# Optimization experiments

Measured on AMD Instinct MI355X. Metric: run time of the kernel, lower is better.

## Reference

```python
import jax, jax.numpy as jnp
import numpy as np

N_NODE = 50000
N_EDGE = 640000
IN_DIM = 128
OUT_DIM = 128
ATTN_DIM = 128
N_REL = 500
REL_VOCAB = 2 * N_REL + 3  # 1003


def setup_inputs() -> dict:
    key = jax.random.key(0)
    ks = jax.random.split(key, 10)
    hidden = jax.random.normal(ks[0], (N_NODE, IN_DIM), dtype=jnp.float32)
    sub = jax.random.randint(ks[1], (N_EDGE,), 0, N_NODE)
    rel = jax.random.randint(ks[2], (N_EDGE,), 0, REL_VOCAB)
    obj = jax.random.randint(ks[3], (N_EDGE,), 0, N_NODE)
    zero = jnp.zeros((N_EDGE,), dtype=jnp.int64 if jax.config.read('jax_enable_x64') else jnp.int32)
    # edges layout: [:,2]=rel, [:,4]=sub, [:,5]=obj (other columns unused)
    edges = jnp.stack([zero, zero, rel, zero, sub, obj], axis=1)
    old_nodes_new_idx = jax.random.randint(ks[4], (N_NODE,), 0, N_NODE)
    s = 1.0 / np.sqrt(IN_DIM)
    rela_embed = jax.random.normal(ks[5], (REL_VOCAB, IN_DIM), dtype=jnp.float32)
    Ws_attn = jax.random.uniform(ks[6], (IN_DIM, ATTN_DIM), minval=-s, maxval=s, dtype=jnp.float32)
    Wr_attn = jax.random.uniform(ks[7], (IN_DIM, ATTN_DIM), minval=-s, maxval=s, dtype=jnp.float32)
    sa = 1.0 / np.sqrt(ATTN_DIM)
    w_alpha_w = jax.random.uniform(ks[8], (ATTN_DIM, 1), minval=-sa, maxval=sa, dtype=jnp.float32)
    w_alpha_b = jnp.zeros((1,), dtype=jnp.float32)
    W_h = jax.random.uniform(ks[9], (IN_DIM, OUT_DIM), minval=-s, maxval=s, dtype=jnp.float32)
    return {
        'hidden': hidden, 'edges': edges, 'n_node': N_NODE,
        'old_nodes_new_idx': old_nodes_new_idx,
        'rela_embed': rela_embed, 'Ws_attn': Ws_attn, 'Wr_attn': Wr_attn,
        'w_alpha_w': w_alpha_w, 'w_alpha_b': w_alpha_b, 'W_h': W_h,
    }


def reference(hidden, edges, n_node, old_nodes_new_idx,
              rela_embed, Ws_attn, Wr_attn, w_alpha_w, w_alpha_b, W_h):
    sub = edges[:, 4]
    rel = edges[:, 2]
    obj = edges[:, 5]
    hs = hidden[sub]                 # [E, in_dim] gather
    hr = rela_embed[rel]             # [E, in_dim] gather
    message = hs + hr                # [E, in_dim]
    attn_h = jax.nn.relu(hs @ Ws_attn + hr @ Wr_attn)          # [E, attn_dim]
    alpha = jax.nn.sigmoid(attn_h @ w_alpha_w + w_alpha_b)     # [E, 1]
    message = alpha * message
    message_agg = jax.ops.segment_sum(message, obj, num_segments=n_node)  # [N, in_dim]
    hidden_new = message_agg @ W_h   # act is identity by default
    return hidden_new
```

## Files before the change

### kernel.cpp

```cpp
#include <hip/hip_runtime.h>

typedef float f4 __attribute__((ext_vector_type(4)));
typedef float f2 __attribute__((ext_vector_type(2)));
typedef float f8 __attribute__((ext_vector_type(8)));
typedef float f32x4 __attribute__((ext_vector_type(4)));
typedef short bf16x8 __attribute__((ext_vector_type(8)));
typedef unsigned short u16x8 __attribute__((ext_vector_type(8)));

__device__ inline float bf2f(unsigned short u) {
  return __uint_as_float(((unsigned)u) << 16);
}
__device__ inline unsigned short f2bf(float f) {
  unsigned u = __float_as_uint(f);
  return (unsigned short)((u + 0x7FFF + ((u >> 16) & 1)) >> 16);
}

__global__ __launch_bounds__(256) void prep(
    const float* __restrict__ Ws, const float* __restrict__ Wr,
    const float* __restrict__ Wh, const int* __restrict__ edges, int n_edge,
    unsigned short* __restrict__ WsT, unsigned short* __restrict__ WrT,
    unsigned short* __restrict__ WhT, int* __restrict__ counts) {
  const int t = threadIdx.x;
  int b = blockIdx.x;
  if (b < 192) {
    int wsel = b >> 6;
    const float* W = wsel == 0 ? Ws : (wsel == 1 ? Wr : Wh);
    unsigned short* WT = wsel == 0 ? WsT : (wsel == 1 ? WrT : WhT);
    int e = (b & 63) * 256 + t;
    int cc = e >> 7, kk = e & 127;
    WT[e] = f2bf(W[kk * 128 + cc]);
    return;
  }
  b -= 192;
  int e = b * 256 + t;
  if (e < n_edge) atomicAdd(&counts[edges[e * 6 + 5]], 1);
}

__global__ __launch_bounds__(256) void gemm_dual(
    const float* __restrict__ hidden, int M, int nbN,
    const float* __restrict__ rela, int relv,
    const unsigned short* __restrict__ WsT, const unsigned short* __restrict__ WrT,
    const unsigned short* __restrict__ WhT,
    char* __restrict__ rec, char* __restrict__ relrec) {
  __shared__ __align__(16) char lds[81920];
  const int t = threadIdx.x;
  int b = blockIdx.x;
  const float* src;
  const unsigned short* WxT;
  char* out;
  int rows, row0;
  if (b < nbN) { src = hidden; WxT = WsT; out = rec; rows = M; row0 = b * 64; }
  else { src = rela; WxT = WrT; out = relrec; rows = relv; row0 = (b - nbN) * 64; }

#pragma unroll
  for (int i = 0; i < 8; ++i) {
    int m = i * 256 + t;
    int sw = (m * 16) ^ (((m >> 4) & 7) << 4);
    *(u16x8*)(lds + 16384 + sw) = ((const u16x8*)WxT)[m];
    *(u16x8*)(lds + 49152 + sw) = ((const u16x8*)WhT)[m];
  }
#pragma unroll
  for (int i = 0; i < 4; ++i) {
    int m = i * 256 + t;
    int r = m >> 4, c = m & 15;
    int gr = row0 + r;
    if (gr > rows - 1) gr = rows - 1;
    const float* s = src + (size_t)gr * 128 + c * 8;
    f4 lo = *(const f4*)s, hi = *(const f4*)(s + 4);
    u16x8 v;
    v[0] = f2bf(lo.x); v[1] = f2bf(lo.y); v[2] = f2bf(lo.z); v[3] = f2bf(lo.w);
    v[4] = f2bf(hi.x); v[5] = f2bf(hi.y); v[6] = f2bf(hi.z); v[7] = f2bf(hi.w);
    *(u16x8*)(lds + ((m * 16) ^ ((r & 7) << 4))) = v;
  }
  __syncthreads();

  const int w = t >> 6, l = t & 63, lr = l & 15, lg = l >> 4;
  const int rowA = w * 16 + lr;
  bf16x8 afr[4];
#pragma unroll
  for (int k0 = 0; k0 < 4; ++k0)
    afr[k0] = *(const bf16x8*)(lds + rowA * 256 + ((k0 * 64 + lg * 16) ^ ((rowA & 7) << 4)));

  {
    f32x4 acc[8] = {};
#pragma unroll
    for (int k0 = 0; k0 < 4; ++k0) {
      int kb = k0 * 64 + lg * 16;
#pragma unroll
      for (int c0 = 0; c0 < 8; ++c0) {
        int cr = c0 * 16 + lr;
        bf16x8 bfr = *(const bf16x8*)(lds + 16384 + cr * 256 + (kb ^ ((cr & 7) << 4)));
        acc[c0] = __builtin_amdgcn_mfma_f32_16x16x32_bf16(afr[k0], bfr, acc[c0], 0, 0, 0);
      }
    }
#pragma unroll
    for (int c0 = 0; c0 < 8; ++c0) {
      int col = c0 * 16 + lr;
#pragma unroll
      for (int j = 0; j < 4; ++j) {
        int grow = row0 + w * 16 + lg * 4 + j;
        if (grow < rows) {
          unsigned pk = __builtin_amdgcn_cvt_pk_fp8_f32(acc[c0][j], acc[c0][j], 0, false);
          *(unsigned char*)(out + (size_t)grow * 384 + 256 + col) = (unsigned char)pk;
        }
      }
    }
  }
  {
    f32x4 acc[8] = {};
#pragma unroll
    for (int k0 = 0; k0 < 4; ++k0) {
      int kb = k0 * 64 + lg * 16;
#pragma unroll
      for (int c0 = 0; c0 < 8; ++c0) {
        int cr = c0 * 16 + lr;
        bf16x8 bfr = *(const bf16x8*)(lds + 49152 + cr * 256 + (kb ^ ((cr & 7) << 4)));
        acc[c0] = __builtin_amdgcn_mfma_f32_16x16x32_bf16(afr[k0], bfr, acc[c0], 0, 0, 0);
      }
    }
#pragma unroll
    for (int c0 = 0; c0 < 8; ++c0) {
      int col = c0 * 16 + lr;
#pragma unroll
      for (int j = 0; j < 4; ++j) {
        int grow = row0 + w * 16 + lg * 4 + j;
        if (grow < rows)
          *(unsigned short*)(out + (size_t)grow * 384 + col * 2) = f2bf(acc[c0][j]);
      }
    }
  }
}

__global__ __launch_bounds__(256) void scan_lookback(
    const int* __restrict__ counts, int M, int n_edge, int* __restrict__ status,
    int* __restrict__ offsets, int* __restrict__ cursor) {
  const int t = threadIdx.x, b = blockIdx.x;
  const int idx = b * 256 + t;
  int c = (idx < M) ? counts[idx] : 0;
  const int lane = t & 63, w = t >> 6;
  int s = c;
  for (int off = 1; off < 64; off <<= 1) {
    int o = __shfl_up(s, off, 64);
    if (lane >= off) s += o;
  }
  __shared__ int wsum[4], wpre[4];
  __shared__ int blk_prefix;
  if (lane == 63) wsum[w] = s;
  __syncthreads();
  if (t == 0) {
    int r = 0;
#pragma unroll
    for (int i = 0; i < 4; ++i) { wpre[i] = r; r += wsum[i]; }
    unsigned pub = ((b == 0 ? 2u : 1u) << 30) | (unsigned)r;
    __hip_atomic_store(&status[b], (int)pub, __ATOMIC_RELEASE, __HIP_MEMORY_SCOPE_AGENT);
    if (b == 0) blk_prefix = 0;
  }
  __syncthreads();
  if (b > 0 && w == 0) {
    int prefix = 0;
    int k = b - 1;
    for (;;) {
      int j = k - lane;
      unsigned v;
      if (j >= 0) {
        do {
          v = (unsigned)__hip_atomic_load(&status[j], __ATOMIC_ACQUIRE,
                                          __HIP_MEMORY_SCOPE_AGENT);
        } while ((v >> 30) == 0u);
      } else {
        v = 2u << 30;
      }
      int val = (int)(v & 0x3FFFFFFFu);
      unsigned long long incl = __ballot((v >> 30) == 2u);
      int l = (int)__ffsll(incl) - 1;
      int contrib = (l >= 0) ? ((lane <= l) ? val : 0) : val;
#pragma unroll
      for (int off = 32; off; off >>= 1) contrib += __shfl_xor(contrib, off, 64);
      prefix += contrib;
      if (l >= 0) break;
      k -= 64;
    }
    if (lane == 0) {
      blk_prefix = prefix;
      int total = wpre[3] + wsum[3];
      __hip_atomic_store(&status[b], (int)((2u << 30) | (unsigned)(prefix + total)),
                         __ATOMIC_RELEASE, __HIP_MEMORY_SCOPE_AGENT);
    }
  }
  __syncthreads();
  int excl = blk_prefix + wpre[w] + s - c;
  if (idx < M) { offsets[idx] = excl; cursor[idx] = excl; }
  if (idx == 0) offsets[M] = n_edge;
}

__global__ __launch_bounds__(256) void scatter_kernel(const int* __restrict__ edges,
                                                      int n_edge, int* __restrict__ cursor,
                                                      uint2* __restrict__ esr2) {
  int e = blockIdx.x * 256 + threadIdx.x;
  if (e < n_edge) {
    int rel = edges[(size_t)e * 6 + 2];
    int2 so = *(const int2*)(edges + (size_t)e * 6 + 4);
    int pos = atomicAdd(&cursor[so.y], 1);
    esr2[pos] = make_uint2((unsigned)(so.x * 384), (unsigned)(rel * 384));
  }
}

__device__ inline float edge_alpha16(uint2 as, uint2 ar, const f8& wa, float bb) {
  f2 a0 = __builtin_amdgcn_cvt_pk_f32_fp8(as.x, false);
  f2 a1 = __builtin_amdgcn_cvt_pk_f32_fp8(as.x, true);
  f2 a2 = __builtin_amdgcn_cvt_pk_f32_fp8(as.y, false);
  f2 a3 = __builtin_amdgcn_cvt_pk_f32_fp8(as.y, true);
  f2 r0 = __builtin_amdgcn_cvt_pk_f32_fp8(ar.x, false);
  f2 r1 = __builtin_amdgcn_cvt_pk_f32_fp8(ar.x, true);
  f2 r2 = __builtin_amdgcn_cvt_pk_f32_fp8(ar.y, false);
  f2 r3 = __builtin_amdgcn_cvt_pk_f32_fp8(ar.y, true);
  float p = fmaxf(a0.x + r0.x, 0.f) * wa[0] + fmaxf(a0.y + r0.y, 0.f) * wa[1] +
            fmaxf(a1.x + r1.x, 0.f) * wa[2] + fmaxf(a1.y + r1.y, 0.f) * wa[3] +
            fmaxf(a2.x + r2.x, 0.f) * wa[4] + fmaxf(a2.y + r2.y, 0.f) * wa[5] +
            fmaxf(a3.x + r3.x, 0.f) * wa[6] + fmaxf(a3.y + r3.y, 0.f) * wa[7];
#pragma unroll
  for (int off = 1; off <= 8; off <<= 1) p += __shfl_xor(p, off, 64);
  return __builtin_amdgcn_rcpf(1.f + __builtin_amdgcn_exp2f(-(p + bb)));
}

__device__ inline f8 msg8(u16x8 h, u16x8 r) {
  f8 m;
#pragma unroll
  for (int j = 0; j < 8; ++j)
    m[j] = bf2f((unsigned short)h[j]) + bf2f((unsigned short)r[j]);
  return m;
}

__global__ __launch_bounds__(256) void node_agg(
    const int* __restrict__ offsets, const uint2* __restrict__ esr2,
    const char* __restrict__ rec, const char* __restrict__ relrec,
    float* __restrict__ out,
    const float* __restrict__ w_alpha, const float* __restrict__ w_b, int M) {
  const int lane = threadIdx.x & 63;
  const int g = lane >> 4, gl = lane & 15;
  const int n = (int)((blockIdx.x * 256u + threadIdx.x) >> 6);
  if (n >= M) return;
  const unsigned bH = gl * 16u, bA = 256u + gl * 8u;
  const float LOG2E = 1.44269504f;
  f8 wa;
  {
    f4 lo = ((const f4*)w_alpha)[gl * 2], hi = ((const f4*)w_alpha)[gl * 2 + 1];
    wa[0] = lo.x; wa[1] = lo.y; wa[2] = lo.z; wa[3] = lo.w;
    wa[4] = hi.x; wa[5] = hi.y; wa[6] = hi.z; wa[7] = hi.w;
    wa *= LOG2E;
  }
  const float bb = w_b[0] * LOG2E;
  const int beg = offsets[n], end = offsets[n + 1];
  f8 acc = {0.f, 0.f, 0.f, 0.f, 0.f, 0.f, 0.f, 0.f};

  for (int i = beg + g; i < end; i += 8) {
    const bool has2 = (i + 4) < end;
    uint2 o1 = esr2[i];
    uint2 o2 = has2 ? esr2[i + 4] : o1;

    u16x8 h1 = *(const u16x8*)(rec + o1.x + bH);
    uint2 as1 = *(const uint2*)(rec + o1.x + bA);
    u16x8 r1 = *(const u16x8*)(relrec + o1.y + bH);
    uint2 ar1 = *(const uint2*)(relrec + o1.y + bA);
    u16x8 h2 = *(const u16x8*)(rec + o2.x + bH);
    uint2 as2 = *(const uint2*)(rec + o2.x + bA);
    u16x8 r2 = *(const u16x8*)(relrec + o2.y + bH);
    uint2 ar2 = *(const uint2*)(relrec + o2.y + bA);

    float alpha1 = edge_alpha16(as1, ar1, wa, bb);
    float alpha2 = edge_alpha16(as2, ar2, wa, bb);
    if (!has2) alpha2 = 0.f;

    acc += alpha1 * msg8(h1, r1);
    acc += alpha2 * msg8(h2, r2);
  }

#pragma unroll
  for (int j = 0; j < 8; ++j) {
    acc[j] += __shfl_xor(acc[j], 16, 64);
    acc[j] += __shfl_xor(acc[j], 32, 64);
  }
  if (g == 0) {
    f4 lo = {acc[0], acc[1], acc[2], acc[3]};
    f4 hi = {acc[4], acc[5], acc[6], acc[7]};
    float* dst = out + (size_t)n * 128 + gl * 8;
    *(f4*)dst = lo;
    *(f4*)(dst + 4) = hi;
  }
}

extern "C" void kernel_launch(void* const* d_in, const int* in_sizes, int n_in,
                              void* d_out, int out_size, void* d_ws, size_t ws_size,
                              hipStream_t stream) {
  const float* hidden = (const float*)d_in[0];
  const int* edges = (const int*)d_in[1];
  const float* rela = (const float*)d_in[4];
  const float* Ws = (const float*)d_in[5];
  const float* Wr = (const float*)d_in[6];
  const float* wa = (const float*)d_in[7];
  const float* wb = (const float*)d_in[8];
  const float* Wh = (const float*)d_in[9];

  const int M = in_sizes[0] / 128;
  const int n_edge = in_sizes[1] / 6;
  const int relv = in_sizes[4] / 128;
  const int NB = (M + 255) / 256;
  const int BE = (n_edge + 255) / 256;

  char* ws = (char*)d_ws;
  size_t off = 0;
  char* rec = ws; off += ((size_t)M * 384 + 255) & ~255ull;
  char* relrec = ws + off; off += ((size_t)relv * 384 + 255) & ~255ull;
  unsigned short* WsT = (unsigned short*)(ws + off); off += 32768;
  unsigned short* WrT = (unsigned short*)(ws + off); off += 32768;
  unsigned short* WhT = (unsigned short*)(ws + off); off += 32768;
  uint2* esr2 = (uint2*)(ws + off); off += (size_t)n_edge * 8;
  int* counts = (int*)(ws + off); off += (size_t)M * 4;
  int* status = (int*)(ws + off); off += 4096;
  int* offsets = (int*)(ws + off); off += ((size_t)(M + 1) * 4 + 255) & ~255ull;
  int* cursor = (int*)(ws + off);
  float* out = (float*)d_out;

  hipMemsetAsync(counts, 0, (size_t)M * 4 + 4096, stream);

  prep<<<192 + BE, 256, 0, stream>>>(Ws, Wr, Wh, edges, n_edge, WsT, WrT, WhT, counts);

  const int nbN = (M + 63) / 64;
  gemm_dual<<<nbN + (relv + 63) / 64, 256, 0, stream>>>(hidden, M, nbN, rela, relv,
                                                        WsT, WrT, WhT, rec, relrec);

  scan_lookback<<<NB, 256, 0, stream>>>(counts, M, n_edge, status, offsets, cursor);
  scatter_kernel<<<BE, 256, 0, stream>>>(edges, n_edge, cursor, esr2);

  node_agg<<<(M * 64 + 255) / 256, 256, 0, stream>>>(offsets, esr2, rec, relrec,
                                                     out, wa, wb, M);
}
```

Before: 152.4 us.

## Pack edge indices in prep and split node edge ranges contiguously per subgroup

The prep kernel now writes a compact 8-byte packed edge record (sub, rel, obj), so the scatter kernel reads that instead of re-gathering from the strided 24-byte edge rows. node_agg splits each node's edge list into contiguous per-subgroup ranges and processes four edges per iteration, issuing more independent gathers per iteration for memory-level parallelism. It also uses packed f2 math for the alpha dot product and the bf16 message unpack. This adds an extra n_edge*8 workspace buffer and one extra write pass, and packing relies on sub fitting in 17 bits and rel in 15 bits.

```diff
diff --git a/kernel.cpp b/kernel.cpp
--- a/kernel.cpp
+++ b/kernel.cpp
@@ -2,14 +2,10 @@
 
 typedef float f4 __attribute__((ext_vector_type(4)));
 typedef float f2 __attribute__((ext_vector_type(2)));
-typedef float f8 __attribute__((ext_vector_type(8)));
 typedef float f32x4 __attribute__((ext_vector_type(4)));
 typedef short bf16x8 __attribute__((ext_vector_type(8)));
 typedef unsigned short u16x8 __attribute__((ext_vector_type(8)));
 
-__device__ inline float bf2f(unsigned short u) {
-  return __uint_as_float(((unsigned)u) << 16);
-}
 __device__ inline unsigned short f2bf(float f) {
   unsigned u = __float_as_uint(f);
   return (unsigned short)((u + 0x7FFF + ((u >> 16) & 1)) >> 16);
@@ -19,7 +15,8 @@
     const float* __restrict__ Ws, const float* __restrict__ Wr,
     const float* __restrict__ Wh, const int* __restrict__ edges, int n_edge,
     unsigned short* __restrict__ WsT, unsigned short* __restrict__ WrT,
-    unsigned short* __restrict__ WhT, int* __restrict__ counts) {
+    unsigned short* __restrict__ WhT, int* __restrict__ counts,
+    uint2* __restrict__ epk) {
   const int t = threadIdx.x;
   int b = blockIdx.x;
   if (b < 192) {
@@ -33,7 +30,12 @@
   }
   b -= 192;
   int e = b * 256 + t;
-  if (e < n_edge) atomicAdd(&counts[edges[e * 6 + 5]], 1);
+  if (e < n_edge) {
+    int rel = edges[(size_t)e * 6 + 2];
+    int2 so = *(const int2*)(edges + (size_t)e * 6 + 4);
+    atomicAdd(&counts[so.y], 1);
+    epk[e] = make_uint2((unsigned)so.x | ((unsigned)rel << 17), (unsigned)so.y);
+  }
 }
 
 __global__ __launch_bounds__(256) void gemm_dual(
@@ -193,42 +195,21 @@
   if (idx == 0) offsets[M] = n_edge;
 }
 
-__global__ __launch_bounds__(256) void scatter_kernel(const int* __restrict__ edges,
+__global__ __launch_bounds__(256) void scatter_kernel(const uint2* __restrict__ epk,
                                                       int n_edge, int* __restrict__ cursor,
                                                       uint2* __restrict__ esr2) {
   int e = blockIdx.x * 256 + threadIdx.x;
   if (e < n_edge) {
-    int rel = edges[(size_t)e * 6 + 2];
-    int2 so = *(const int2*)(edges + (size_t)e * 6 + 4);
-    int pos = atomicAdd(&cursor[so.y], 1);
-    esr2[pos] = make_uint2((unsigned)(so.x * 384), (unsigned)(rel * 384));
-  }
-}
-
-__device__ inline float edge_alpha16(uint2 as, uint2 ar, const f8& wa, float bb) {
-  f2 a0 = __builtin_amdgcn_cvt_pk_f32_fp8(as.x, false);
-  f2 a1 = __builtin_amdgcn_cvt_pk_f32_fp8(as.x, true);
-  f2 a2 = __builtin_amdgcn_cvt_pk_f32_fp8(as.y, false);
-  f2 a3 = __builtin_amdgcn_cvt_pk_f32_fp8(as.y, true);
-  f2 r0 = __builtin_amdgcn_cvt_pk_f32_fp8(ar.x, false);
-  f2 r1 = __builtin_amdgcn_cvt_pk_f32_fp8(ar.x, true);
-  f2 r2 = __builtin_amdgcn_cvt_pk_f32_fp8(ar.y, false);
-  f2 r3 = __builtin_amdgcn_cvt_pk_f32_fp8(ar.y, true);
-  float p = fmaxf(a0.x + r0.x, 0.f) * wa[0] + fmaxf(a0.y + r0.y, 0.f) * wa[1] +
-            fmaxf(a1.x + r1.x, 0.f) * wa[2] + fmaxf(a1.y + r1.y, 0.f) * wa[3] +
-            fmaxf(a2.x + r2.x, 0.f) * wa[4] + fmaxf(a2.y + r2.y, 0.f) * wa[5] +
-            fmaxf(a3.x + r3.x, 0.f) * wa[6] + fmaxf(a3.y + r3.y, 0.f) * wa[7];
-#pragma unroll
-  for (int off = 1; off <= 8; off <<= 1) p += __shfl_xor(p, off, 64);
-  return __builtin_amdgcn_rcpf(1.f + __builtin_amdgcn_exp2f(-(p + bb)));
-}
-
-__device__ inline f8 msg8(u16x8 h, u16x8 r) {
-  f8 m;
-#pragma unroll
-  for (int j = 0; j < 8; ++j)
-    m[j] = bf2f((unsigned short)h[j]) + bf2f((unsigned short)r[j]);
-  return m;
+    uint2 pe = epk[e];
+    int pos = atomicAdd(&cursor[pe.y], 1);
+    unsigned sub = pe.x & 0x1FFFF, rel = pe.x >> 17;
+    esr2[pos] = make_uint2(sub * 384u, rel * 384u);
+  }
+}
+
+template <bool HI>
+__device__ inline f2 pk8(unsigned u) {
+  return __builtin_amdgcn_cvt_pk_f32_fp8(u, HI);
 }
 
 __global__ __launch_bounds__(256) void node_agg(
@@ -242,47 +223,83 @@
   if (n >= M) return;
   const unsigned bH = gl * 16u, bA = 256u + gl * 8u;
   const float LOG2E = 1.44269504f;
-  f8 wa;
-  {
-    f4 lo = ((const f4*)w_alpha)[gl * 2], hi = ((const f4*)w_alpha)[gl * 2 + 1];
-    wa[0] = lo.x; wa[1] = lo.y; wa[2] = lo.z; wa[3] = lo.w;
-    wa[4] = hi.x; wa[5] = hi.y; wa[6] = hi.z; wa[7] = hi.w;
-    wa *= LOG2E;
-  }
+  f2 wap[4];
+#pragma unroll
+  for (int k = 0; k < 4; ++k) wap[k] = ((const f2*)w_alpha)[gl * 4 + k] * LOG2E;
   const float bb = w_b[0] * LOG2E;
+
   const int beg = offsets[n], end = offsets[n + 1];
-  f8 acc = {0.f, 0.f, 0.f, 0.f, 0.f, 0.f, 0.f, 0.f};
-
-  for (int i = beg + g; i < end; i += 8) {
-    const bool has2 = (i + 4) < end;
-    uint2 o1 = esr2[i];
-    uint2 o2 = has2 ? esr2[i + 4] : o1;
-
-    u16x8 h1 = *(const u16x8*)(rec + o1.x + bH);
-    uint2 as1 = *(const uint2*)(rec + o1.x + bA);
-    u16x8 r1 = *(const u16x8*)(relrec + o1.y + bH);
-    uint2 ar1 = *(const uint2*)(relrec + o1.y + bA);
-    u16x8 h2 = *(const u16x8*)(rec + o2.x + bH);
-    uint2 as2 = *(const uint2*)(rec + o2.x + bA);
-    u16x8 r2 = *(const u16x8*)(relrec + o2.y + bH);
-    uint2 ar2 = *(const uint2*)(relrec + o2.y + bA);
-
-    float alpha1 = edge_alpha16(as1, ar1, wa, bb);
-    float alpha2 = edge_alpha16(as2, ar2, wa, bb);
-    if (!has2) alpha2 = 0.f;
-
-    acc += alpha1 * msg8(h1, r1);
-    acc += alpha2 * msg8(h2, r2);
-  }
-
-#pragma unroll
-  for (int j = 0; j < 8; ++j) {
-    acc[j] += __shfl_xor(acc[j], 16, 64);
-    acc[j] += __shfl_xor(acc[j], 32, 64);
+  const int len = end - beg;
+  const int q = len >> 2, rem = len & 3;
+  const int gbeg = beg + g * q + min(g, rem);
+  const int gend = gbeg + q + (g < rem ? 1 : 0);
+
+  f2 acc2[4] = {};
+
+  for (int j = gbeg; j < gend; j += 4) {
+    const int jm = gend - 1;
+    uint2 o[4];
+#pragma unroll
+    for (int s = 0; s < 4; ++s) {
+      int jj = j + s;
+      o[s] = esr2[jj > jm ? jm : jj];
+    }
+    u16x8 h[4], r[4];
+    uint2 as[4], ar[4];
+#pragma unroll
+    for (int s = 0; s < 4; ++s) {
+      h[s] = *(const u16x8*)(rec + o[s].x + bH);
+      as[s] = *(const uint2*)(rec + o[s].x + bA);
+      r[s] = *(const u16x8*)(relrec + o[s].y + bH);
+      ar[s] = *(const uint2*)(relrec + o[s].y + bA);
+    }
+    float al[4];
+#pragma unroll
+    for (int s = 0; s < 4; ++s) {
+      f2 s0 = pk8<false>(as[s].x) + pk8<false>(ar[s].x);
+      f2 s1 = pk8<true>(as[s].x) + pk8<true>(ar[s].x);
+      f2 s2 = pk8<false>(as[s].y) + pk8<false>(ar[s].y);
+      f2 s3 = pk8<true>(as[s].y) + pk8<true>(ar[s].y);
+      s0.x = fmaxf(s0.x, 0.f); s0.y = fmaxf(s0.y, 0.f);
+      s1.x = fmaxf(s1.x, 0.f); s1.y = fmaxf(s1.y, 0.f);
+      s2.x = fmaxf(s2.x, 0.f); s2.y = fmaxf(s2.y, 0.f);
+      s3.x = fmaxf(s3.x, 0.f); s3.y = fmaxf(s3.y, 0.f);
+      f2 pp = s0 * wap[0];
+      pp += s1 * wap[1];
+      pp += s2 * wap[2];
+      pp += s3 * wap[3];
+      float p = pp.x + pp.y;
+#pragma unroll
+      for (int off = 1; off <= 8; off <<= 1) p += __shfl_xor(p, off, 64);
+      float a = __builtin_amdgcn_rcpf(1.f + __builtin_amdgcn_exp2f(-(p + bb)));
+      al[s] = (j + s <= jm) ? a : 0.f;
+    }
+#pragma unroll
+    for (int s = 0; s < 4; ++s) {
+      const uint4 hu = *(const uint4*)&h[s];
+      const uint4 ru = *(const uint4*)&r[s];
+      const unsigned hd[4] = {hu.x, hu.y, hu.z, hu.w};
+      const unsigned rd[4] = {ru.x, ru.y, ru.z, ru.w};
+#pragma unroll
+      for (int k = 0; k < 4; ++k) {
+        f2 m;
+        m.x = __uint_as_float(hd[k] << 16) + __uint_as_float(rd[k] << 16);
+        m.y = __uint_as_float(hd[k] & 0xFFFF0000u) + __uint_as_float(rd[k] & 0xFFFF0000u);
+        acc2[k] += al[s] * m;
+      }
+    }
+  }
+
+#pragma unroll
+  for (int k = 0; k < 4; ++k) {
+    acc2[k].x += __shfl_xor(acc2[k].x, 16, 64);
+    acc2[k].y += __shfl_xor(acc2[k].y, 16, 64);
+    acc2[k].x += __shfl_xor(acc2[k].x, 32, 64);
+    acc2[k].y += __shfl_xor(acc2[k].y, 32, 64);
   }
   if (g == 0) {
-    f4 lo = {acc[0], acc[1], acc[2], acc[3]};
-    f4 hi = {acc[4], acc[5], acc[6], acc[7]};
+    f4 lo = {acc2[0].x, acc2[0].y, acc2[1].x, acc2[1].y};
+    f4 hi = {acc2[2].x, acc2[2].y, acc2[3].x, acc2[3].y};
     float* dst = out + (size_t)n * 128 + gl * 8;
     *(f4*)dst = lo;
     *(f4*)(dst + 4) = hi;
@@ -315,22 +332,24 @@
   unsigned short* WrT = (unsigned short*)(ws + off); off += 32768;
   unsigned short* WhT = (unsigned short*)(ws + off); off += 32768;
   uint2* esr2 = (uint2*)(ws + off); off += (size_t)n_edge * 8;
+  uint2* epk = (uint2*)(ws + off); off += (size_t)n_edge * 8;
   int* counts = (int*)(ws + off); off += (size_t)M * 4;
   int* status = (int*)(ws + off); off += 4096;
   int* offsets = (int*)(ws + off); off += ((size_t)(M + 1) * 4 + 255) & ~255ull;
   int* cursor = (int*)(ws + off);
   float* out = (float*)d_out;
 
-  hipMemsetAsync(counts, 0, (size_t)M * 4 + 4096, stream);
-
-  prep<<<192 + BE, 256, 0, stream>>>(Ws, Wr, Wh, edges, n_edge, WsT, WrT, WhT, counts);
+  (void)hipMemsetAsync(counts, 0, (size_t)M * 4 + 4096, stream);
+
+  prep<<<192 + BE, 256, 0, stream>>>(Ws, Wr, Wh, edges, n_edge, WsT, WrT, WhT,
+                                     counts, epk);
 
   const int nbN = (M + 63) / 64;
   gemm_dual<<<nbN + (relv + 63) / 64, 256, 0, stream>>>(hidden, M, nbN, rela, relv,
                                                         WsT, WrT, WhT, rec, relrec);
 
   scan_lookback<<<NB, 256, 0, stream>>>(counts, M, n_edge, status, offsets, cursor);
-  scatter_kernel<<<BE, 256, 0, stream>>>(edges, n_edge, cursor, esr2);
+  scatter_kernel<<<BE, 256, 0, stream>>>(epk, n_edge, cursor, esr2);
 
   node_agg<<<(M * 64 + 255) / 256, 256, 0, stream>>>(offsets, esr2, rec, relrec,
                                                      out, wa, wb, M);
```

Result: slower. 175.6 us (+15.2%).
